# Kernel optimization log

Hardware: AMD Instinct MI355X
Metric: run time of the kernel (lower is better)

## Reference

```python
import jax, jax.numpy as jnp
import numpy as np

N = 50000   # nodes
E = 800000  # edges
D = 128     # input feature dim
H = 128     # hidden dim
L = 3       # num GIN layers
G = 64      # graphs in batch


def setup_inputs() -> dict:
    key = jax.random.key(0)
    ks = jax.random.split(key, 20)
    inp = {
        "h": jax.random.normal(ks[0], (N, D), jnp.float32),
        "src": jax.random.randint(ks[1], (E,), 0, N),
        "dst": jax.random.randint(ks[2], (E,), 0, N),
        "graph_ids": jnp.sort(jax.random.randint(ks[3], (N,), 0, G)),
    }
    k = 4
    for i in range(L):
        in_dim = D if i == 0 else H
        inp[f"w1_{i}"] = jax.random.normal(ks[k], (in_dim, H), jnp.float32) / np.sqrt(in_dim).astype(np.float32); k += 1
        inp[f"b1_{i}"] = jnp.zeros((H,), jnp.float32)
        inp[f"w2_{i}"] = jax.random.normal(ks[k], (H, H), jnp.float32) / np.sqrt(H).astype(np.float32); k += 1
        inp[f"b2_{i}"] = jnp.zeros((H,), jnp.float32)
    inp["w_out"] = jax.random.normal(ks[k], (H * L, 1), jnp.float32) / np.sqrt(H * L).astype(np.float32)
    inp["b_out"] = jnp.zeros((1,), jnp.float32)
    return inp


def _gin_layer(h, src, dst, w1, b1, w2, b2):
    # sum aggregation over edges: agg[i] = sum_{(j->i) in E} h[j]
    agg = jax.ops.segment_sum(h[src], dst, num_segments=N)
    z = h + agg  # (1 + eps) * h + agg with eps = 0 (DGL GINConv default)
    return jax.nn.relu(z @ w1 + b1) @ w2 + b2  # 2-layer MLP


def reference(h, src, dst, graph_ids,
              w1_0, b1_0, w2_0, b2_0,
              w1_1, b1_1, w2_1, b2_1,
              w1_2, b1_2, w2_2, b2_2,
              w_out, b_out):
    layers = [(w1_0, b1_0, w2_0, b2_0),
              (w1_1, b1_1, w2_1, b2_1),
              (w1_2, b1_2, w2_2, b2_2)]
    readouts = []
    for w1, b1, w2, b2 in layers:
        h = _gin_layer(h, src, dst, w1, b1, w2, b2)
        # per-graph sum readout of node features: [G, H]
        readouts.append(jax.ops.segment_sum(h, graph_ids, num_segments=G))
    hg = jnp.concatenate(readouts, axis=1)  # [G, H*L]
    return hg @ w_out + b_out  # [G, 1]
```

## Files before the change

### kernel.cpp

```cpp
#include <hip/hip_runtime.h>

#define NN 50000
#define NE 800000
#define DIMH 128
#define NGRAPH 64
#define NTILES 3125
#define MLP_BLOCKS 782
#define NBIN 196
#define BCAP 8064

typedef __attribute__((ext_vector_type(8))) short bf16x8;
typedef __attribute__((ext_vector_type(4))) float f32x4;

__device__ __forceinline__ unsigned short f2b(float f) {
  unsigned int b = __float_as_uint(f);
  unsigned int r = (b + 0x7FFFu + ((b >> 16) & 1u)) >> 16;
  return (unsigned short)r;
}
__device__ __forceinline__ float b2f_lo(unsigned int u) { return __uint_as_float(u << 16); }
__device__ __forceinline__ float b2f_hi(unsigned int u) { return __uint_as_float(u & 0xffff0000u); }


__global__ void zero_int_kernel(int* __restrict__ p, int n) {
  int i = blockIdx.x * 256 + threadIdx.x;
  if (i < n) p[i] = 0;
}

__global__ __launch_bounds__(256) void bin_scatter_kernel(const int* __restrict__ src,
                                                          const int* __restrict__ dst,
                                                          int* __restrict__ gcnt,
                                                          int2* __restrict__ staging) {
  __shared__ int hist[NBIN];
  __shared__ int base[NBIN];
  int tid = threadIdx.x;
  for (int i = tid; i < NBIN; i += 256) hist[i] = 0;
  __syncthreads();
  int e0 = blockIdx.x * 2048;
  int2 ed[8];
  int bin[8], rank[8];
#pragma unroll
  for (int k = 0; k < 8; ++k) {
    int e = e0 + k * 256 + tid;
    bin[k] = 0; rank[k] = 0; ed[k] = make_int2(0, 0);
    if (e < NE) {
      ed[k].x = src[e]; ed[k].y = dst[e];
      bin[k] = ed[k].y >> 8;
      rank[k] = atomicAdd(&hist[bin[k]], 1);
    }
  }
  __syncthreads();
  for (int i = tid; i < NBIN; i += 256) base[i] = atomicAdd(&gcnt[i], hist[i]);
  __syncthreads();
#pragma unroll
  for (int k = 0; k < 8; ++k) {
    int e = e0 + k * 256 + tid;
    if (e < NE) staging[bin[k] * BCAP + base[bin[k]] + rank[k]] = ed[k];
  }
}

__global__ __launch_bounds__(256) void bin_fill_kernel(const int2* __restrict__ staging,
                                                       const int* __restrict__ gcnt,
                                                       int* __restrict__ bucket,
                                                       int* __restrict__ cnt) {
  __shared__ int h[256];
  int b = blockIdx.x;
  int tid = threadIdx.x;
  h[tid] = 0;
  __syncthreads();
  int n = gcnt[b];
  for (int i = tid; i < n; i += 256) {
    int2 e = staging[b * BCAP + i];
    int local = e.y & 255;
    int r = atomicAdd(&h[local], 1);
    if (r < 64) bucket[(b * 256 + local) * 64 + r] = e.x;
  }
  __syncthreads();
  int node = b * 256 + tid;
  if (node < NN) cnt[node] = h[tid];
}


__global__ void convw_kernel(const float* __restrict__ w, unsigned short* __restrict__ wt) {
  int i = blockIdx.x * 256 + threadIdx.x;
  int c = i >> 7, k = i & 127;
  wt[i] = f2b(w[k * DIMH + c]);
}

__global__ void convh_kernel(const float* __restrict__ h, unsigned int* __restrict__ o) {
  int i = blockIdx.x * 256 + threadIdx.x;
  float2 v = ((const float2*)h)[i];
  o[i] = (unsigned int)f2b(v.x) | ((unsigned int)f2b(v.y) << 16);
}


__global__ void agg_kernel(const uint2* __restrict__ hp, const int* __restrict__ cnt,
                           const int* __restrict__ bucket, uint2* __restrict__ z) {
  int gidx = blockIdx.x * 256 + threadIdx.x;
  int node = gidx >> 6;
  int lane = gidx & 63;
  int half = lane >> 5;
  int l5 = lane & 31;
  int c = cnt[node];
  if (c > 64) c = 64;
  int idx = bucket[node * 64 + lane];

  uint2 own = hp[node * 32 + l5];
  float a0 = b2f_lo(own.x), a1 = b2f_hi(own.x), a2 = b2f_lo(own.y), a3 = b2f_hi(own.y);
  if (half) { a0 = 0.f; a1 = 0.f; a2 = 0.f; a3 = 0.f; }

  int j = 0;
  for (; j + 8 <= c; j += 8) {
#pragma unroll
    for (int k = 0; k < 4; ++k) {
      int nb = __shfl(idx, j + 2 * k + half, 64);
      uint2 u = hp[nb * 32 + l5];
      a0 += b2f_lo(u.x); a1 += b2f_hi(u.x);
      a2 += b2f_lo(u.y); a3 += b2f_hi(u.y);
    }
  }
  for (; j < c; j += 2) {
    int slot = j + half;
    int s2 = slot < c ? slot : 0;
    int nb = __shfl(idx, s2, 64);
    uint2 u = hp[nb * 32 + l5];
    float m = slot < c ? 1.f : 0.f;
    a0 += m * b2f_lo(u.x); a1 += m * b2f_hi(u.x);
    a2 += m * b2f_lo(u.y); a3 += m * b2f_hi(u.y);
  }

  a0 += __shfl_xor(a0, 32, 64);
  a1 += __shfl_xor(a1, 32, 64);
  a2 += __shfl_xor(a2, 32, 64);
  a3 += __shfl_xor(a3, 32, 64);

  if (half == 0) {
    uint2 o;
    o.x = (unsigned int)f2b(a0) | ((unsigned int)f2b(a1) << 16);
    o.y = (unsigned int)f2b(a2) | ((unsigned int)f2b(a3) << 16);
    z[node * 32 + l5] = o;
  }
}

__global__ __launch_bounds__(256) void mlp_kernel(const unsigned short* __restrict__ X,
                                                  const unsigned short* __restrict__ W1t,
                                                  const float* __restrict__ b1,
                                                  const unsigned short* __restrict__ W2t,
                                                  const float* __restrict__ b2,
                                                  unsigned short* __restrict__ Y,
                                                  const int* __restrict__ gids,
                                                  const float* __restrict__ wout,
                                                  float* __restrict__ gout) {
  __shared__ unsigned short y1[4][2048];
  __shared__ float s_gout[NGRAPH];
  int tid = threadIdx.x;
  if (tid < NGRAPH) s_gout[tid] = 0.f;
  __syncthreads();

  int wv = tid >> 6;
  int lane = tid & 63;
  int l15 = lane & 15;
  int g = lane >> 4;
  int rt = blockIdx.x * 4 + wv;

  if (rt < NTILES) {
    int row0 = rt * 16;
    const unsigned short* xbase = X + (row0 + l15) * DIMH + g * 8;
    bf16x8 a[4];
#pragma unroll
    for (int kt = 0; kt < 4; ++kt) a[kt] = *(const bf16x8*)(xbase + kt * 32);

    unsigned short* yt = y1[wv];
    const unsigned short* w1base = W1t + l15 * DIMH + g * 8;
#pragma unroll
    for (int n = 0; n < 8; ++n) {
      f32x4 acc = (f32x4){0.f, 0.f, 0.f, 0.f};
#pragma unroll
      for (int kt = 0; kt < 4; ++kt) {
        bf16x8 bfr = *(const bf16x8*)(w1base + n * 16 * DIMH + kt * 32);
        acc = __builtin_amdgcn_mfma_f32_16x16x32_bf16(a[kt], bfr, acc, 0, 0, 0);
      }
      float bv = b1[n * 16 + l15];
      int col2 = (n * 16 + l15) * 2;
#pragma unroll
      for (int r = 0; r < 4; ++r) {
        float f = fmaxf(acc[r] + bv, 0.f);
        int row = 4 * g + r;
        yt[((row * 256 + col2) ^ (row << 4)) >> 1] = f2b(f);
      }
    }

    bf16x8 a2[4];
#pragma unroll
    for (int kt = 0; kt < 4; ++kt)
      a2[kt] = *(const bf16x8*)&yt[((l15 * 256 + kt * 64 + g * 16) ^ (l15 << 4)) >> 1];

    float p[4] = {0.f, 0.f, 0.f, 0.f};
    const unsigned short* w2base = W2t + l15 * DIMH + g * 8;
#pragma unroll
    for (int n = 0; n < 8; ++n) {
      f32x4 acc = (f32x4){0.f, 0.f, 0.f, 0.f};
#pragma unroll
      for (int kt = 0; kt < 4; ++kt) {
        bf16x8 bfr = *(const bf16x8*)(w2base + n * 16 * DIMH + kt * 32);
        acc = __builtin_amdgcn_mfma_f32_16x16x32_bf16(a2[kt], bfr, acc, 0, 0, 0);
      }
      int col = n * 16 + l15;
      float bv = b2[col];
      float wv2 = wout[col];
#pragma unroll
      for (int r = 0; r < 4; ++r) {
        float f = acc[r] + bv;
        if (Y) Y[(row0 + 4 * g + r) * DIMH + col] = f2b(f);
        p[r] += f * wv2;
      }
    }

#pragma unroll
    for (int r = 0; r < 4; ++r) {
#pragma unroll
      for (int off = 1; off < 16; off <<= 1) p[r] += __shfl_xor(p[r], off, 64);
    }
    if (l15 == 0) {
#pragma unroll
      for (int r = 0; r < 4; ++r)
        atomicAdd(&s_gout[gids[row0 + 4 * g + r]], p[r]);
    }
  }

  __syncthreads();
  if (tid < NGRAPH) {
    float v = s_gout[tid];
    if (v != 0.f) atomicAdd(&gout[tid], v);
  }
}

__global__ void init_out_kernel(float* __restrict__ out, const float* __restrict__ b_out) {
  int i = threadIdx.x;
  if (i < NGRAPH) out[i] = b_out[0];
}


extern "C" void kernel_launch(void* const* d_in, const int* in_sizes, int n_in,
                              void* d_out, int out_size, void* d_ws, size_t ws_size,
                              hipStream_t stream) {
  const float* h = (const float*)d_in[0];
  const int* src = (const int*)d_in[1];
  const int* dst = (const int*)d_in[2];
  const int* gids = (const int*)d_in[3];
  const float* w_out = (const float*)d_in[16];
  const float* b_out = (const float*)d_in[17];
  float* out = (float*)d_out;

  char* base = (char*)d_ws;
  unsigned int* bufH = (unsigned int*)(base);
  int2* staging = (int2*)(base + 12800000);
  unsigned int* bufC = (unsigned int*)(base + 25600000);
  int* bucket = (int*)(base + 38400000);
  int* cnt = (int*)(base + 51200000);
  int* gcnt = (int*)(base + 51400000);
  unsigned short* wt = (unsigned short*)(base + 51401024);

  zero_int_kernel<<<1, 256, 0, stream>>>(gcnt, NBIN);
  bin_scatter_kernel<<<(NE + 2047) / 2048, 256, 0, stream>>>(src, dst, gcnt, staging);
  bin_fill_kernel<<<NBIN, 256, 0, stream>>>(staging, gcnt, bucket, cnt);

  for (int l = 0; l < 3; ++l) {
    convw_kernel<<<64, 256, 0, stream>>>((const float*)d_in[4 + l * 4], wt + (2 * l) * 16384);
    convw_kernel<<<64, 256, 0, stream>>>((const float*)d_in[6 + l * 4], wt + (2 * l + 1) * 16384);
  }
  convh_kernel<<<(NN * 64) / 256, 256, 0, stream>>>(h, bufH);

  init_out_kernel<<<1, 64, 0, stream>>>(out, b_out);

  int agg_blocks = (NN * 64) / 256;

  for (int l = 0; l < 3; ++l) {
    const float* b1 = (const float*)d_in[5 + l * 4];
    const float* b2 = (const float*)d_in[7 + l * 4];
    const unsigned short* w1t = wt + (2 * l) * 16384;
    const unsigned short* w2t = wt + (2 * l + 1) * 16384;

    agg_kernel<<<agg_blocks, 256, 0, stream>>>((const uint2*)bufH, cnt, bucket, (uint2*)bufC);
    mlp_kernel<<<MLP_BLOCKS, 256, 0, stream>>>((const unsigned short*)bufC, w1t, b1, w2t, b2,
                                               (l == 2) ? nullptr : (unsigned short*)bufH,
                                               gids, w_out + l * DIMH, out);
  }
}
```

Before: 253.3 us.

## Make MLP kernel persistent with register-resident weights and paired-wave tiles

The MLP kernel now runs a fixed grid of blocks. Each pair of waves shares a 16-row tile, and each wave computes half of the output columns. Both weight halves are loaded into registers once and reused across four tile iterations, which removes the repeated global weight fetches each tile used to do. The next tile's input is prefetched while the current one computes, and the LDS hidden buffer is double-buffered with a block-wide barrier per iteration. In exchange, register pressure rises sharply (launch bounds of 256 threads with 2 blocks), which may limit occupancy or cause spills.

```diff
diff --git a/kernel.cpp b/kernel.cpp
--- a/kernel.cpp
+++ b/kernel.cpp
@@ -5,7 +5,9 @@
 #define DIMH 128
 #define NGRAPH 64
 #define NTILES 3125
-#define MLP_BLOCKS 782
+#define PAIRS 1024
+#define MLP_BLOCKS 512
+#define MLP_ITERS 4
 #define NBIN 196
 #define BCAP 8064
 
@@ -141,89 +143,118 @@
   }
 }
 
-__global__ __launch_bounds__(256) void mlp_kernel(const unsigned short* __restrict__ X,
-                                                  const unsigned short* __restrict__ W1t,
-                                                  const float* __restrict__ b1,
-                                                  const unsigned short* __restrict__ W2t,
-                                                  const float* __restrict__ b2,
-                                                  unsigned short* __restrict__ Y,
-                                                  const int* __restrict__ gids,
-                                                  const float* __restrict__ wout,
-                                                  float* __restrict__ gout) {
-  __shared__ unsigned short y1[4][2048];
+__global__ __launch_bounds__(256, 2) void mlp_kernel(const unsigned short* __restrict__ X,
+                                                     const unsigned short* __restrict__ W1t,
+                                                     const float* __restrict__ b1,
+                                                     const unsigned short* __restrict__ W2t,
+                                                     const float* __restrict__ b2,
+                                                     unsigned short* __restrict__ Y,
+                                                     const int* __restrict__ gids,
+                                                     const float* __restrict__ wout,
+                                                     float* __restrict__ gout) {
+  __shared__ unsigned short y1[2][2][2048];
   __shared__ float s_gout[NGRAPH];
   int tid = threadIdx.x;
   if (tid < NGRAPH) s_gout[tid] = 0.f;
-  __syncthreads();
 
   int wv = tid >> 6;
   int lane = tid & 63;
+  int pb = wv >> 1;
+  int half = wv & 1;
   int l15 = lane & 15;
   int g = lane >> 4;
-  int rt = blockIdx.x * 4 + wv;
-
-  if (rt < NTILES) {
-    int row0 = rt * 16;
-    const unsigned short* xbase = X + (row0 + l15) * DIMH + g * 8;
-    bf16x8 a[4];
-#pragma unroll
-    for (int kt = 0; kt < 4; ++kt) a[kt] = *(const bf16x8*)(xbase + kt * 32);
-
-    unsigned short* yt = y1[wv];
-    const unsigned short* w1base = W1t + l15 * DIMH + g * 8;
-#pragma unroll
-    for (int n = 0; n < 8; ++n) {
-      f32x4 acc = (f32x4){0.f, 0.f, 0.f, 0.f};
-#pragma unroll
-      for (int kt = 0; kt < 4; ++kt) {
-        bf16x8 bfr = *(const bf16x8*)(w1base + n * 16 * DIMH + kt * 32);
-        acc = __builtin_amdgcn_mfma_f32_16x16x32_bf16(a[kt], bfr, acc, 0, 0, 0);
+  int p = blockIdx.x * 2 + pb;
+
+  bf16x8 a[4];
+  {
+    const unsigned short* xb = X + (p * 16 + l15) * DIMH + g * 8;
+#pragma unroll
+    for (int kt = 0; kt < 4; ++kt) a[kt] = *(const bf16x8*)(xb + kt * 32);
+  }
+
+  bf16x8 fb1[4][4], fb2[4][4];
+  const unsigned short* w1b = W1t + (half * 64 + l15) * DIMH + g * 8;
+  const unsigned short* w2b = W2t + (half * 64 + l15) * DIMH + g * 8;
+#pragma unroll
+  for (int n = 0; n < 4; ++n)
+#pragma unroll
+    for (int kt = 0; kt < 4; ++kt) {
+      fb1[n][kt] = *(const bf16x8*)(w1b + n * 16 * DIMH + kt * 32);
+      fb2[n][kt] = *(const bf16x8*)(w2b + n * 16 * DIMH + kt * 32);
+    }
+  float b1v[4], b2v[4], wov[4];
+#pragma unroll
+  for (int n = 0; n < 4; ++n) {
+    int col = half * 64 + n * 16 + l15;
+    b1v[n] = b1[col];
+    b2v[n] = b2[col];
+    wov[n] = wout[col];
+  }
+  __syncthreads();
+
+#pragma unroll
+  for (int i = 0; i < MLP_ITERS; ++i) {
+    int rtc = p + i * PAIRS;
+    bool active = rtc < NTILES;
+    unsigned short* buf = y1[pb][i & 1];
+
+    if (active) {
+#pragma unroll
+      for (int n = 0; n < 4; ++n) {
+        f32x4 acc = (f32x4){0.f, 0.f, 0.f, 0.f};
+#pragma unroll
+        for (int kt = 0; kt < 4; ++kt)
+          acc = __builtin_amdgcn_mfma_f32_16x16x32_bf16(a[kt], fb1[n][kt], acc, 0, 0, 0);
+        int col2 = (half * 64 + n * 16 + l15) * 2;
+#pragma unroll
+        for (int r = 0; r < 4; ++r) {
+          float f = fmaxf(acc[r] + b1v[n], 0.f);
+          int row = 4 * g + r;
+          buf[((row * 256 + col2) ^ (row << 4)) >> 1] = f2b(f);
+        }
       }
-      float bv = b1[n * 16 + l15];
-      int col2 = (n * 16 + l15) * 2;
+    }
+
+    int rtn = p + (i + 1) * PAIRS;
+    if (i + 1 < MLP_ITERS && rtn < NTILES) {
+      const unsigned short* xb = X + (rtn * 16 + l15) * DIMH + g * 8;
+#pragma unroll
+      for (int kt = 0; kt < 4; ++kt) a[kt] = *(const bf16x8*)(xb + kt * 32);
+    }
+
+    __syncthreads();
+
+    if (active) {
+      bf16x8 a2[4];
+#pragma unroll
+      for (int kt = 0; kt < 4; ++kt)
+        a2[kt] = *(const bf16x8*)&buf[((l15 * 256 + kt * 64 + g * 16) ^ (l15 << 4)) >> 1];
+
+      float pr[4] = {0.f, 0.f, 0.f, 0.f};
+#pragma unroll
+      for (int n = 0; n < 4; ++n) {
+        f32x4 acc = (f32x4){0.f, 0.f, 0.f, 0.f};
+#pragma unroll
+        for (int kt = 0; kt < 4; ++kt)
+          acc = __builtin_amdgcn_mfma_f32_16x16x32_bf16(a2[kt], fb2[n][kt], acc, 0, 0, 0);
+        int col = half * 64 + n * 16 + l15;
+#pragma unroll
+        for (int r = 0; r < 4; ++r) {
+          float f = acc[r] + b2v[n];
+          if (Y) Y[(rtc * 16 + 4 * g + r) * DIMH + col] = f2b(f);
+          pr[r] += f * wov[n];
+        }
+      }
 #pragma unroll
       for (int r = 0; r < 4; ++r) {
-        float f = fmaxf(acc[r] + bv, 0.f);
-        int row = 4 * g + r;
-        yt[((row * 256 + col2) ^ (row << 4)) >> 1] = f2b(f);
+#pragma unroll
+        for (int off = 1; off < 16; off <<= 1) pr[r] += __shfl_xor(pr[r], off, 64);
       }
-    }
-
-    bf16x8 a2[4];
-#pragma unroll
-    for (int kt = 0; kt < 4; ++kt)
-      a2[kt] = *(const bf16x8*)&yt[((l15 * 256 + kt * 64 + g * 16) ^ (l15 << 4)) >> 1];
-
-    float p[4] = {0.f, 0.f, 0.f, 0.f};
-    const unsigned short* w2base = W2t + l15 * DIMH + g * 8;
-#pragma unroll
-    for (int n = 0; n < 8; ++n) {
-      f32x4 acc = (f32x4){0.f, 0.f, 0.f, 0.f};
-#pragma unroll
-      for (int kt = 0; kt < 4; ++kt) {
-        bf16x8 bfr = *(const bf16x8*)(w2base + n * 16 * DIMH + kt * 32);
-        acc = __builtin_amdgcn_mfma_f32_16x16x32_bf16(a2[kt], bfr, acc, 0, 0, 0);
+      if (l15 == 0) {
+#pragma unroll
+        for (int r = 0; r < 4; ++r)
+          atomicAdd(&s_gout[gids[rtc * 16 + 4 * g + r]], pr[r]);
       }
-      int col = n * 16 + l15;
-      float bv = b2[col];
-      float wv2 = wout[col];
-#pragma unroll
-      for (int r = 0; r < 4; ++r) {
-        float f = acc[r] + bv;
-        if (Y) Y[(row0 + 4 * g + r) * DIMH + col] = f2b(f);
-        p[r] += f * wv2;
-      }
-    }
-
-#pragma unroll
-    for (int r = 0; r < 4; ++r) {
-#pragma unroll
-      for (int off = 1; off < 16; off <<= 1) p[r] += __shfl_xor(p[r], off, 64);
-    }
-    if (l15 == 0) {
-#pragma unroll
-      for (int r = 0; r < 4; ++r)
-        atomicAdd(&s_gout[gids[row0 + 4 * g + r]], p[r]);
     }
   }
 
```

After: 214.0 us. 15.5% less time.
